# Performance work log

Hardware: AMD Instinct MI355X
Metric: run time of the kernel (lower is better)

## Reference

```python
import jax, jax.numpy as jnp
import numpy as np

B, P, E = 64, 196, 2048      # batch, num_pixels (14*14), encoder_size
H, EMB, V = 512, 512, 10000  # hidden_size, embed_size, vocab_size
T_CAP = 50                   # hard-coded pred/alpha buffer length
T_MAX = T_CAP - 1            # max(decode_lengths) = max(lengths) - 1 = 49


def setup_inputs() -> dict:
    key = jax.random.key(0)
    ks = jax.random.split(key, 20)

    def lin(k, out_f, in_f):
        kw, kb = jax.random.split(k)
        s = 1.0 / np.sqrt(in_f)
        return (jax.random.uniform(kw, (out_f, in_f), jnp.float32, -s, s),
                jax.random.uniform(kb, (out_f,), jnp.float32, -s, s))

    features = jax.random.normal(ks[0], (B, P, E), jnp.float32)
    captions = jax.random.randint(ks[1], (B, T_CAP), 0, V)
    # sorted descending, first length forced to 50 so max(decode_lengths)=49
    lengths = jnp.sort(jax.random.randint(ks[2], (B,), 2, T_CAP + 1))[::-1]
    lengths = lengths.at[0].set(T_CAP)

    Wx_w, Wx_b = lin(ks[3], E, E)          # attention Wx: encoder->encoder
    Wh_w, Wh_b = lin(ks[4], E, H)          # attention Wh: hidden->encoder
    V_w, V_b = lin(ks[5], 1, E)            # attention V: encoder->1
    init_h_w, init_h_b = lin(ks[6], H, E)  # init_h
    f_beta_w, f_beta_b = lin(ks[7], E, H)  # f_beta gate
    embed_w = jax.random.normal(ks[8], (V, EMB), jnp.float32)
    gru_w_ih, gru_b_ih = lin(ks[9], 3 * H, E + EMB)
    gru_w_hh, gru_b_hh = lin(ks[10], 3 * H, H)
    fc1_w, fc1_b = lin(ks[11], V, H)

    return dict(features=features, captions=captions, lengths=lengths,
                Wx_w=Wx_w, Wx_b=Wx_b, Wh_w=Wh_w, Wh_b=Wh_b, V_w=V_w, V_b=V_b,
                init_h_w=init_h_w, init_h_b=init_h_b,
                f_beta_w=f_beta_w, f_beta_b=f_beta_b, embed_w=embed_w,
                gru_w_ih=gru_w_ih, gru_b_ih=gru_b_ih,
                gru_w_hh=gru_w_hh, gru_b_hh=gru_b_hh,
                fc1_w=fc1_w, fc1_b=fc1_b)


def reference(features, captions, lengths, Wx_w, Wx_b, Wh_w, Wh_b, V_w, V_b,
              init_h_w, init_h_b, f_beta_w, f_beta_b, embed_w,
              gru_w_ih, gru_b_ih, gru_w_hh, gru_b_hh, fc1_w, fc1_b):
    b, p, e = features.shape
    vsz = fc1_w.shape[0]
    dec = lengths - 1                                  # decode_lengths
    # init hidden state from mean-pooled features
    h0 = jnp.mean(features, axis=1) @ init_h_w.T + init_h_b      # [B,H]
    # Wx(features) is time-invariant: precompute once
    x_wx = jnp.einsum('bpe,fe->bpf', features, Wx_w) + Wx_b      # [B,P,E]
    emb = embed_w[captions]                                      # [B,50,EMB]
    emb_t = jnp.transpose(emb[:, :T_MAX], (1, 0, 2))             # [T,B,EMB]

    def step(h, xs):
        t, e_t = xs
        active = (dec >= t)                            # rows still decoding
        # Bahdanau attention
        h_wh = h @ Wh_w.T + Wh_b                       # [B,E]
        lam = jnp.einsum('bpe,oe->bpo',
                         jnp.tanh(x_wx + h_wh[:, None, :]), V_w) + V_b
        alpha = jax.nn.softmax(lam, axis=1)            # [B,P,1]
        z = jnp.sum(alpha * features, axis=1)          # [B,E]
        # sigmoid gate
        gate = jax.nn.sigmoid(h @ f_beta_w.T + f_beta_b)
        inp = jnp.concatenate([gate * z, e_t], axis=1)  # [B,E+EMB]
        # GRUCell (torch gate order r,z,n)
        gi = inp @ gru_w_ih.T + gru_b_ih
        gh = h @ gru_w_hh.T + gru_b_hh
        i_r, i_z, i_n = jnp.split(gi, 3, axis=-1)
        h_r, h_z, h_n = jnp.split(gh, 3, axis=-1)
        r = jax.nn.sigmoid(i_r + h_r)
        zg = jax.nn.sigmoid(i_z + h_z)
        n = jnp.tanh(i_n + r * h_n)
        h_new = (1.0 - zg) * n + zg * h
        pred = h_new @ fc1_w.T + fc1_b                 # dropout in eval = id
        m = active[:, None]
        h_out = jnp.where(m, h_new, h)                 # freeze finished rows
        return h_out, (jnp.where(m, pred, 0.0),
                       jnp.where(m, alpha[..., 0], 0.0))

    _, (preds_t, alphas_t) = jax.lax.scan(
        step, h0, (jnp.arange(T_MAX), emb_t))
    preds = jnp.zeros((b, T_CAP, vsz), features.dtype)
    preds = preds.at[:, :T_MAX].set(jnp.transpose(preds_t, (1, 0, 2)))
    alphas = jnp.zeros((b, T_CAP, p), features.dtype)
    alphas = alphas.at[:, :T_MAX].set(jnp.transpose(alphas_t, (1, 0, 2)))
    return preds, alphas, dec
```

## Files before the change

### kernel.cpp

```cpp
#include <hip/hip_runtime.h>
#include <cstddef>

#define B_    64
#define P_    196
#define E_    2048
#define H_    512
#define EMB_  512
#define V_    10000
#define TCAP_ 50
#define TMAX_ 49
#define KI_   2560
#define G3_   1536

typedef __attribute__((ext_vector_type(8))) short short8;
typedef __attribute__((ext_vector_type(4))) float floatx4;
typedef unsigned int u32;
typedef const __attribute__((address_space(1))) u32* gptr_t;
typedef __attribute__((address_space(3))) u32* lptr_t;

__device__ __forceinline__ unsigned short f2bf_rne(float f) {
    unsigned int x = __float_as_uint(f);
    unsigned int r = (x + 0x7fffu + ((x >> 16) & 1u)) >> 16;
    return (unsigned short)r;
}
__device__ __forceinline__ float bf2f(unsigned int u16) {
    return __uint_as_float(u16 << 16);
}
__device__ __forceinline__ float fast_tanh(float x) {
    float a = fabsf(x);
    float e = __expf(2.0f * a);
    float r = 1.0f - 2.0f / (e + 1.0f);
    return (x < 0.0f) ? -r : r;
}
__device__ __forceinline__ float fast_sig(float x) {
    return 1.0f / (1.0f + __expf(-x));
}

__global__ void init_out_kernel(float* __restrict__ preds, float* __restrict__ alphas,
                                float* __restrict__ dec, const int* __restrict__ lens)
{
    int i = blockIdx.x * 256 + threadIdx.x;
    if (i < B_ * V_) {
        int b = i / V_, v = i - b * V_;
        preds[((size_t)b * TCAP_ + TMAX_) * V_ + v] = 0.f;
    }
    if (i < B_ * P_) {
        int b = i / P_, p = i - b * P_;
        alphas[((size_t)b * TCAP_ + TMAX_) * P_ + p] = 0.f;
    }
    if (i < B_) dec[i] = (float)(lens[i] - 1);
}

__global__ void f2bf_kernel(const float* __restrict__ src, unsigned short* __restrict__ dst, int n8)
{
    int i = blockIdx.x * 256 + threadIdx.x;
    if (i >= n8) return;
    float4 a = ((const float4*)src)[2 * i];
    float4 b = ((const float4*)src)[2 * i + 1];
    uint4 o;
    o.x = (unsigned)f2bf_rne(a.x) | ((unsigned)f2bf_rne(a.y) << 16);
    o.y = (unsigned)f2bf_rne(a.z) | ((unsigned)f2bf_rne(a.w) << 16);
    o.z = (unsigned)f2bf_rne(b.x) | ((unsigned)f2bf_rne(b.y) << 16);
    o.w = (unsigned)f2bf_rne(b.z) | ((unsigned)f2bf_rne(b.w) << 16);
    ((uint4*)dst)[i] = o;
}

__global__ void mean_kernel(const float* __restrict__ f, unsigned short* __restrict__ out)
{
    int i = blockIdx.x * 256 + threadIdx.x;
    int b = i >> 11, e = i & 2047;
    const float* p = f + (size_t)b * P_ * E_ + e;
    float s = 0.f;
    #pragma unroll 4
    for (int k = 0; k < P_; ++k) s += p[(size_t)k * E_];
    out[i] = f2bf_rne(s * (1.0f / (float)P_));
}

__global__ void __launch_bounds__(256)
mfma_xwx_kernel(const unsigned short* __restrict__ A,
                const unsigned short* __restrict__ W,
                const float* __restrict__ bias,
                unsigned short* __restrict__ C)
{
    __shared__ unsigned short As[128 * 64];
    __shared__ unsigned short Bs[128 * 64];
    int wv = threadIdx.x >> 6, lane = threadIdx.x & 63;
    int mr = lane & 15, quad = lane >> 4;
    int m0 = blockIdx.y * 128;
    int n0 = blockIdx.x * 128;
    int wm = (wv & 1) * 64, wn = (wv >> 1) * 64;
    int srow = wv * 32;
    int lrow = lane >> 3;
    int lcol = (lane & 7) * 8;
    floatx4 acc[4][4] = {};
    for (int k0 = 0; k0 < E_; k0 += 64) {
        __syncthreads();
        #pragma unroll
        for (int i = 0; i < 4; ++i) {
            int r = srow + i * 8;
            __builtin_amdgcn_global_load_lds(
                (gptr_t)(A + (size_t)(m0 + r + lrow) * E_ + k0 + lcol),
                (lptr_t)(As + r * 64), 16, 0, 0);
            __builtin_amdgcn_global_load_lds(
                (gptr_t)(W + (size_t)(n0 + r + lrow) * E_ + k0 + lcol),
                (lptr_t)(Bs + r * 64), 16, 0, 0);
        }
        __syncthreads();
        #pragma unroll
        for (int kk = 0; kk < 64; kk += 32) {
            short8 af[4], bf[4];
            #pragma unroll
            for (int i = 0; i < 4; ++i)
                af[i] = *(const short8*)(As + (wm + i * 16 + mr) * 64 + kk + quad * 8);
            #pragma unroll
            for (int j = 0; j < 4; ++j)
                bf[j] = *(const short8*)(Bs + (wn + j * 16 + mr) * 64 + kk + quad * 8);
            #pragma unroll
            for (int i = 0; i < 4; ++i)
                #pragma unroll
                for (int j = 0; j < 4; ++j)
                    acc[i][j] = __builtin_amdgcn_mfma_f32_16x16x32_bf16(af[i], bf[j], acc[i][j], 0, 0, 0);
        }
    }
    #pragma unroll
    for (int j = 0; j < 4; ++j) {
        int col = n0 + wn + j * 16 + mr;
        float bs = bias[col];
        #pragma unroll
        for (int i = 0; i < 4; ++i) {
            int row = m0 + wm + i * 16 + quad * 4;
            #pragma unroll
            for (int ii = 0; ii < 4; ++ii)
                C[(size_t)(row + ii) * E_ + col] = f2bf_rne(acc[i][j][ii] + bs);
        }
    }
}

template<int KC>
__global__ void __launch_bounds__(256)
mfma_gemm64(const unsigned short* __restrict__ A, int ld,
            const unsigned short* __restrict__ W,
            const float* __restrict__ bias,
            float* __restrict__ C, unsigned short* __restrict__ Cbf, int ldc)
{
    int wv = threadIdx.x >> 6, lane = threadIdx.x & 63;
    int mr = lane & 15, quad = lane >> 4;
    int m0 = wv * 16;
    int n0 = blockIdx.x * 16;
    const unsigned short* pa = A + (size_t)(m0 + mr) * ld + quad * 8;
    const unsigned short* pb = W + (size_t)(n0 + mr) * ld + quad * 8;
    floatx4 acc = {0.f, 0.f, 0.f, 0.f};
    #pragma unroll 16
    for (int k0 = 0; k0 < KC; k0 += 32) {
        short8 a = *(const short8*)(const void*)(pa + k0);
        short8 b = *(const short8*)(const void*)(pb + k0);
        acc = __builtin_amdgcn_mfma_f32_16x16x32_bf16(a, b, acc, 0, 0, 0);
    }
    int col = n0 + mr;
    float bs = bias ? bias[col] : 0.f;
    #pragma unroll
    for (int i = 0; i < 4; ++i) {
        int row = m0 + quad * 4 + i;
        float v = acc[i] + bs;
        C[(size_t)row * ldc + col] = v;
        if (Cbf) Cbf[(size_t)row * ldc + col] = f2bf_rne(v);
    }
}

__global__ void __launch_bounds__(256)
mfma_h3(const unsigned short* __restrict__ hbf,
        const unsigned short* __restrict__ whbf, const float* __restrict__ Wh_b,
        const unsigned short* __restrict__ fbbf, const float* __restrict__ fb_b,
        const unsigned short* __restrict__ ghhbf, const float* __restrict__ ghh_b,
        float* __restrict__ hwh, float* __restrict__ hf, float* __restrict__ gh)
{
    int bt = blockIdx.x;
    const unsigned short* W; const float* bias; float* C; int n0; int ldc;
    if (bt < 128)      { W = whbf;  bias = Wh_b;  C = hwh; n0 = bt * 16;         ldc = E_; }
    else if (bt < 256) { W = fbbf;  bias = fb_b;  C = hf;  n0 = (bt - 128) * 16; ldc = E_; }
    else               { W = ghhbf; bias = ghh_b; C = gh;  n0 = (bt - 256) * 16; ldc = G3_; }
    int wv = threadIdx.x >> 6, lane = threadIdx.x & 63;
    int mr = lane & 15, quad = lane >> 4;
    int m0 = wv * 16;
    const unsigned short* pa = hbf + (size_t)(m0 + mr) * H_ + quad * 8;
    const unsigned short* pb = W + (size_t)(n0 + mr) * H_ + quad * 8;
    floatx4 acc0 = {0.f, 0.f, 0.f, 0.f};
    floatx4 acc1 = {0.f, 0.f, 0.f, 0.f};
    #pragma unroll
    for (int k0 = 0; k0 < 256; k0 += 32) {
        short8 a0 = *(const short8*)(const void*)(pa + k0);
        short8 b0 = *(const short8*)(const void*)(pb + k0);
        acc0 = __builtin_amdgcn_mfma_f32_16x16x32_bf16(a0, b0, acc0, 0, 0, 0);
        short8 a1 = *(const short8*)(const void*)(pa + k0 + 256);
        short8 b1 = *(const short8*)(const void*)(pb + k0 + 256);
        acc1 = __builtin_amdgcn_mfma_f32_16x16x32_bf16(a1, b1, acc1, 0, 0, 0);
    }
    floatx4 acc = acc0 + acc1;
    int col = n0 + mr;
    float bs = bias[col];
    #pragma unroll
    for (int i = 0; i < 4; ++i) {
        int row = m0 + quad * 4 + i;
        C[(size_t)row * ldc + col] = acc[i] + bs;
    }
}

__global__ void __launch_bounds__(256)
lam_kernel(const unsigned short* __restrict__ xwx, const float* __restrict__ hwh,
           const float* __restrict__ Vw, const float* __restrict__ Vb,
           float* __restrict__ lam)
{
    __shared__ float sh[E_];
    __shared__ float sv[E_];
    int b = blockIdx.y;
    int p0 = blockIdx.x * 16;
    int tid = threadIdx.x;
    {
        const float4* hs = (const float4*)(hwh + (size_t)b * E_);
        const float4* vs = (const float4*)Vw;
        ((float4*)sh)[tid]       = hs[tid];
        ((float4*)sh)[tid + 256] = hs[tid + 256];
        ((float4*)sv)[tid]       = vs[tid];
        ((float4*)sv)[tid + 256] = vs[tid + 256];
    }
    __syncthreads();
    int wv = tid >> 6, lane = tid & 63;
    #pragma unroll
    for (int r = 0; r < 4; ++r) {
        int p = p0 + wv * 4 + r;
        if (p < P_) {
            const unsigned short* px = xwx + ((size_t)b * P_ + p) * E_;
            float acc = 0.f;
            #pragma unroll
            for (int it = 0; it < 4; ++it) {
                int e = it * 512 + lane * 8;
                uint4 u = *(const uint4*)(const void*)(px + e);
                float4 h0 = *(const float4*)(sh + e);
                float4 h1 = *(const float4*)(sh + e + 4);
                float4 v0 = *(const float4*)(sv + e);
                float4 v1 = *(const float4*)(sv + e + 4);
                acc = fmaf(fast_tanh(bf2f(u.x & 0xffffu) + h0.x), v0.x, acc);
                acc = fmaf(fast_tanh(bf2f(u.x >> 16)     + h0.y), v0.y, acc);
                acc = fmaf(fast_tanh(bf2f(u.y & 0xffffu) + h0.z), v0.z, acc);
                acc = fmaf(fast_tanh(bf2f(u.y >> 16)     + h0.w), v0.w, acc);
                acc = fmaf(fast_tanh(bf2f(u.z & 0xffffu) + h1.x), v1.x, acc);
                acc = fmaf(fast_tanh(bf2f(u.z >> 16)     + h1.y), v1.y, acc);
                acc = fmaf(fast_tanh(bf2f(u.w & 0xffffu) + h1.z), v1.z, acc);
                acc = fmaf(fast_tanh(bf2f(u.w >> 16)     + h1.w), v1.w, acc);
            }
            #pragma unroll
            for (int off = 32; off > 0; off >>= 1) acc += __shfl_down(acc, off);
            if (lane == 0) lam[b * P_ + p] = acc + Vb[0];
        }
    }
}

__global__ void __launch_bounds__(256)
attn_z_kernel(const unsigned short* __restrict__ fbf, const float* __restrict__ lam,
              const float* __restrict__ hf, const float* __restrict__ embed_w,
              const int* __restrict__ captions, const int* __restrict__ lens,
              unsigned short* __restrict__ inpbf, float* __restrict__ alphas, int t)
{
    int b = blockIdx.y;
    int tile = blockIdx.x;
    int tid = threadIdx.x;
    if (tile == 4) {
        int cap = captions[b * TCAP_ + t];
        const float* e = embed_w + (size_t)cap * EMB_;
        int c = tid * 2;
        float2 v = *(const float2*)(e + c);
        *(unsigned int*)(inpbf + (size_t)b * KI_ + E_ + c) =
            (unsigned)f2bf_rne(v.x) | ((unsigned)f2bf_rne(v.y) << 16);
        return;
    }
    __shared__ float sa[256];
    __shared__ float sr[256];
    float x = (tid < P_) ? lam[b * P_ + tid] : -1e30f;
    sr[tid] = x;
    __syncthreads();
    for (int s = 128; s > 0; s >>= 1) {
        if (tid < s) sr[tid] = fmaxf(sr[tid], sr[tid + s]);
        __syncthreads();
    }
    float mx = sr[0];
    __syncthreads();
    float ex = (tid < P_) ? __expf(x - mx) : 0.f;
    sa[tid] = ex;
    sr[tid] = ex;
    __syncthreads();
    for (int s = 128; s > 0; s >>= 1) {
        if (tid < s) sr[tid] += sr[tid + s];
        __syncthreads();
    }
    float inv = 1.0f / sr[0];
    if (tile == 0 && tid < P_) {
        alphas[(size_t)b * TCAP_ * P_ + (size_t)t * P_ + tid] = (lens[b] > t) ? ex * inv : 0.f;
    }
    int e0 = tile * 512 + tid * 2;
    const unsigned short* fp = fbf + (size_t)b * P_ * E_ + e0;
    float a0 = 0.f, a1 = 0.f;
    #pragma unroll 4
    for (int p = 0; p < P_; ++p) {
        unsigned int u = *(const unsigned int*)(const void*)(fp + (size_t)p * E_);
        float ap = sa[p];
        a0 = fmaf(ap, bf2f(u & 0xffffu), a0);
        a1 = fmaf(ap, bf2f(u >> 16), a1);
    }
    a0 *= inv; a1 *= inv;
    float2 gv = *(const float2*)(hf + (size_t)b * E_ + e0);
    float g0 = fast_sig(gv.x), g1 = fast_sig(gv.y);
    *(unsigned int*)(inpbf + (size_t)b * KI_ + e0) =
        (unsigned)f2bf_rne(g0 * a0) | ((unsigned)f2bf_rne(g1 * a1) << 16);
}

__global__ void __launch_bounds__(256)
gigru_kernel(const unsigned short* __restrict__ inpbf,
             const unsigned short* __restrict__ wihbf,
             const float* __restrict__ b_ih,
             const float* __restrict__ gh,
             const int* __restrict__ lens,
             float* __restrict__ h, unsigned short* __restrict__ hbf,
             unsigned short* __restrict__ Hall, int t)
{
    __shared__ float red[4][3][16][17];
    int wv = threadIdx.x >> 6, lane = threadIdx.x & 63;
    int mr = lane & 15, quad = lane >> 4;
    int j0 = blockIdx.x * 16;
    int m0 = blockIdx.y * 16;
    int koff = wv * 640;
    const unsigned short* pa = inpbf + (size_t)(m0 + mr) * KI_ + koff + quad * 8;
    const unsigned short* pb0 = wihbf + (size_t)(j0 + mr) * KI_ + koff + quad * 8;
    const unsigned short* pb1 = pb0 + (size_t)512 * KI_;
    const unsigned short* pb2 = pb0 + (size_t)1024 * KI_;
    floatx4 ar = {0.f,0.f,0.f,0.f}, az = {0.f,0.f,0.f,0.f}, an = {0.f,0.f,0.f,0.f};
    #pragma unroll 4
    for (int k0 = 0; k0 < 640; k0 += 32) {
        short8 a = *(const short8*)(const void*)(pa + k0);
        short8 br = *(const short8*)(const void*)(pb0 + k0);
        short8 bz = *(const short8*)(const void*)(pb1 + k0);
        short8 bn = *(const short8*)(const void*)(pb2 + k0);
        ar = __builtin_amdgcn_mfma_f32_16x16x32_bf16(a, br, ar, 0, 0, 0);
        az = __builtin_amdgcn_mfma_f32_16x16x32_bf16(a, bz, az, 0, 0, 0);
        an = __builtin_amdgcn_mfma_f32_16x16x32_bf16(a, bn, an, 0, 0, 0);
    }
    #pragma unroll
    for (int i = 0; i < 4; ++i) {
        red[wv][0][quad * 4 + i][mr] = ar[i];
        red[wv][1][quad * 4 + i][mr] = az[i];
        red[wv][2][quad * 4 + i][mr] = an[i];
    }
    __syncthreads();
    int row = threadIdx.x >> 4, col = threadIdx.x & 15;
    int b = m0 + row, j = j0 + col;
    float ir = red[0][0][row][col] + red[1][0][row][col] + red[2][0][row][col] + red[3][0][row][col] + b_ih[j];
    float iz = red[0][1][row][col] + red[1][1][row][col] + red[2][1][row][col] + red[3][1][row][col] + b_ih[512 + j];
    float in_= red[0][2][row][col] + red[1][2][row][col] + red[2][2][row][col] + red[3][2][row][col] + b_ih[1024 + j];
    float hr = gh[(size_t)b * G3_ + j];
    float hz = gh[(size_t)b * G3_ + 512 + j];
    float hn = gh[(size_t)b * G3_ + 1024 + j];
    float r  = fast_sig(ir + hr);
    float zg = fast_sig(iz + hz);
    float n  = fast_tanh(in_ + r * hn);
    float hp = h[(size_t)b * H_ + j];
    float hv = (1.f - zg) * n + zg * hp;
    float ho = (lens[b] > t) ? hv : hp;
    h[(size_t)b * H_ + j] = ho;
    unsigned short hob = f2bf_rne(ho);
    hbf[(size_t)b * H_ + j] = hob;
    Hall[((size_t)t * B_ + b) * H_ + j] = hob;
}

__global__ void __launch_bounds__(256)
fc1all_kernel(const unsigned short* __restrict__ Hall,
              const unsigned short* __restrict__ W,
              const float* __restrict__ bias,
              float* __restrict__ preds, const int* __restrict__ lens)
{
    int wv = threadIdx.x >> 6, lane = threadIdx.x & 63;
    int mr = lane & 15, quad = lane >> 4;
    int t = blockIdx.x;
    int m0 = t * 64 + wv * 16;
    int n0 = blockIdx.y * 64;
    const unsigned short* pa = Hall + (size_t)(m0 + mr) * H_ + quad * 8;
    const unsigned short* pw0 = W + (size_t)min(n0 + mr, V_ - 1) * H_ + quad * 8;
    const unsigned short* pw1 = W + (size_t)min(n0 + 16 + mr, V_ - 1) * H_ + quad * 8;
    const unsigned short* pw2 = W + (size_t)min(n0 + 32 + mr, V_ - 1) * H_ + quad * 8;
    const unsigned short* pw3 = W + (size_t)min(n0 + 48 + mr, V_ - 1) * H_ + quad * 8;
    floatx4 acc[4] = {{0.f,0.f,0.f,0.f},{0.f,0.f,0.f,0.f},{0.f,0.f,0.f,0.f},{0.f,0.f,0.f,0.f}};
    #pragma unroll
    for (int k0 = 0; k0 < H_; k0 += 32) {
        short8 a = *(const short8*)(const void*)(pa + k0);
        short8 b0 = *(const short8*)(const void*)(pw0 + k0);
        short8 b1 = *(const short8*)(const void*)(pw1 + k0);
        short8 b2 = *(const short8*)(const void*)(pw2 + k0);
        short8 b3 = *(const short8*)(const void*)(pw3 + k0);
        acc[0] = __builtin_amdgcn_mfma_f32_16x16x32_bf16(a, b0, acc[0], 0, 0, 0);
        acc[1] = __builtin_amdgcn_mfma_f32_16x16x32_bf16(a, b1, acc[1], 0, 0, 0);
        acc[2] = __builtin_amdgcn_mfma_f32_16x16x32_bf16(a, b2, acc[2], 0, 0, 0);
        acc[3] = __builtin_amdgcn_mfma_f32_16x16x32_bf16(a, b3, acc[3], 0, 0, 0);
    }
    #pragma unroll
    for (int r = 0; r < 4; ++r) {
        int col = n0 + r * 16 + mr;
        if (col >= V_) continue;
        float bs = bias[col];
        #pragma unroll
        for (int i = 0; i < 4; ++i) {
            int row = m0 + quad * 4 + i;
            int b = row - t * 64;
            float v = (lens[b] > t) ? (acc[r][i] + bs) : 0.f;
            preds[((size_t)b * TCAP_ + t) * V_ + col] = v;
        }
    }
}

extern "C" void kernel_launch(void* const* d_in, const int* in_sizes, int n_in,
                              void* d_out, int out_size, void* d_ws, size_t ws_size,
                              hipStream_t stream)
{
    const float* features  = (const float*)d_in[0];
    const int*   captions  = (const int*)d_in[1];
    const int*   lengths   = (const int*)d_in[2];
    const float* Wx_w      = (const float*)d_in[3];
    const float* Wx_b      = (const float*)d_in[4];
    const float* Wh_w      = (const float*)d_in[5];
    const float* Wh_b      = (const float*)d_in[6];
    const float* V_w       = (const float*)d_in[7];
    const float* V_b       = (const float*)d_in[8];
    const float* init_h_w  = (const float*)d_in[9];
    const float* init_h_b  = (const float*)d_in[10];
    const float* f_beta_w  = (const float*)d_in[11];
    const float* f_beta_b  = (const float*)d_in[12];
    const float* embed_w   = (const float*)d_in[13];
    const float* gru_w_ih  = (const float*)d_in[14];
    const float* gru_b_ih  = (const float*)d_in[15];
    const float* gru_w_hh  = (const float*)d_in[16];
    const float* gru_b_hh  = (const float*)d_in[17];
    const float* fc1_w     = (const float*)d_in[18];
    const float* fc1_b     = (const float*)d_in[19];

    float* preds  = (float*)d_out;
    float* alphas = preds + (size_t)B_ * TCAP_ * V_;
    float* dec    = alphas + (size_t)B_ * TCAP_ * P_;

    char* w = (char*)d_ws;
    unsigned short* fbf     = (unsigned short*)w; w += (size_t)12544 * 2048 * 2;
    unsigned short* xwx     = (unsigned short*)w; w += (size_t)12544 * 2048 * 2;
    unsigned short* wxbf    = (unsigned short*)w; w += (size_t)2048 * 2048 * 2;
    unsigned short* whbf    = (unsigned short*)w; w += (size_t)2048 * 512 * 2;
    unsigned short* fbbf    = (unsigned short*)w; w += (size_t)2048 * 512 * 2;
    unsigned short* ghhbf   = (unsigned short*)w; w += (size_t)1536 * 512 * 2;
    unsigned short* wihbf   = (unsigned short*)w; w += (size_t)1536 * 2560 * 2;
    unsigned short* fc1bf   = (unsigned short*)w; w += (size_t)10000 * 512 * 2;
    unsigned short* ihwbf   = (unsigned short*)w; w += (size_t)512 * 2048 * 2;
    unsigned short* fmeanbf = (unsigned short*)w; w += (size_t)64 * 2048 * 2;
    unsigned short* hbf     = (unsigned short*)w; w += (size_t)64 * 512 * 2;
    unsigned short* inpbf   = (unsigned short*)w; w += (size_t)64 * KI_ * 2;
    unsigned short* Hall    = (unsigned short*)w; w += (size_t)TMAX_ * 64 * 512 * 2;
    float* h   = (float*)w; w += (size_t)64 * 512 * 4;
    float* hwh = (float*)w; w += (size_t)64 * 2048 * 4;
    float* hf  = (float*)w; w += (size_t)64 * 2048 * 4;
    float* gh  = (float*)w; w += (size_t)64 * 1536 * 4;
    float* lam = (float*)w; w += (size_t)64 * 196 * 4;

    init_out_kernel<<<2500, 256, 0, stream>>>(preds, alphas, dec, lengths);

    f2bf_kernel<<<12544, 256, 0, stream>>>(features, fbf, 12544 * 2048 / 8);
    f2bf_kernel<<<2048, 256, 0, stream>>>(Wx_w, wxbf, 2048 * 2048 / 8);
    f2bf_kernel<<<512, 256, 0, stream>>>(Wh_w, whbf, 2048 * 512 / 8);
    f2bf_kernel<<<512, 256, 0, stream>>>(f_beta_w, fbbf, 2048 * 512 / 8);
    f2bf_kernel<<<384, 256, 0, stream>>>(gru_w_hh, ghhbf, 1536 * 512 / 8);
    f2bf_kernel<<<1920, 256, 0, stream>>>(gru_w_ih, wihbf, 1536 * 2560 / 8);
    f2bf_kernel<<<2500, 256, 0, stream>>>(fc1_w, fc1bf, 10000 * 512 / 8);
    f2bf_kernel<<<512, 256, 0, stream>>>(init_h_w, ihwbf, 512 * 2048 / 8);

    mean_kernel<<<512, 256, 0, stream>>>(features, fmeanbf);
    mfma_gemm64<2048><<<32, 256, 0, stream>>>(fmeanbf, 2048, ihwbf, init_h_b, h, hbf, 512);
    mfma_xwx_kernel<<<dim3(16, 98), 256, 0, stream>>>(fbf, wxbf, Wx_b, xwx);

    for (int t = 0; t < TMAX_; ++t) {
        mfma_h3<<<352, 256, 0, stream>>>(hbf, whbf, Wh_b, fbbf, f_beta_b, ghhbf, gru_b_hh,
                                         hwh, hf, gh);
        lam_kernel<<<dim3(13, 64), 256, 0, stream>>>(xwx, hwh, V_w, V_b, lam);
        attn_z_kernel<<<dim3(5, 64), 256, 0, stream>>>(fbf, lam, hf, embed_w, captions,
                                                       lengths, inpbf, alphas, t);
        gigru_kernel<<<dim3(32, 4), 256, 0, stream>>>(inpbf, wihbf, gru_b_ih, gh,
                                                      lengths, h, hbf, Hall, t);
    }
    fc1all_kernel<<<dim3(TMAX_, 157), 256, 0, stream>>>(Hall, fc1bf, fc1_b, preds, lengths);
}
```

Baseline: 4.016 ms.

## Tile fc1 GEMM through LDS and vectorize attention context reduction

Replaces the per-timestep fc1 output GEMM with a 128x128 LDS-tiled MFMA kernel. It stages Hall and fc1 weight tiles with global_load_lds and pads both buffers so out-of-range rows are never read past the allocation. Separately, attn_z now splits the 196 pixels across four waves, uses 16-byte loads of 8 bf16 values, and combines the partial sums through shared memory. Both changes aim to cut redundant global loads and raise memory efficiency. The risk is that the padded rows read whatever the workspace holds, and those values are masked only at the output store.

After: 3.328 ms. 17.1% less time.

```diff
diff --git a/kernel.cpp b/kernel.cpp
--- a/kernel.cpp
+++ b/kernel.cpp
@@ -136,6 +136,72 @@
     }
 }
 
+__global__ void __launch_bounds__(256)
+fc1tile_kernel(const unsigned short* __restrict__ Hall,
+               const unsigned short* __restrict__ W,
+               const float* __restrict__ bias,
+               float* __restrict__ preds, const int* __restrict__ lens)
+{
+    __shared__ unsigned short As[128 * 64];
+    __shared__ unsigned short Bs[128 * 64];
+    int wv = threadIdx.x >> 6, lane = threadIdx.x & 63;
+    int mr = lane & 15, quad = lane >> 4;
+    int m0 = blockIdx.y * 128;
+    int n0 = blockIdx.x * 128;
+    int wm = (wv & 1) * 64, wn = (wv >> 1) * 64;
+    int srow = wv * 32;
+    int lrow = lane >> 3;
+    int lcol = (lane & 7) * 8;
+    floatx4 acc[4][4] = {};
+    for (int k0 = 0; k0 < H_; k0 += 64) {
+        __syncthreads();
+        #pragma unroll
+        for (int i = 0; i < 4; ++i) {
+            int r = srow + i * 8;
+            __builtin_amdgcn_global_load_lds(
+                (gptr_t)(Hall + (size_t)(m0 + r + lrow) * H_ + k0 + lcol),
+                (lptr_t)(As + r * 64), 16, 0, 0);
+            __builtin_amdgcn_global_load_lds(
+                (gptr_t)(W + (size_t)(n0 + r + lrow) * H_ + k0 + lcol),
+                (lptr_t)(Bs + r * 64), 16, 0, 0);
+        }
+        __syncthreads();
+        #pragma unroll
+        for (int kk = 0; kk < 64; kk += 32) {
+            short8 af[4], bf[4];
+            #pragma unroll
+            for (int i = 0; i < 4; ++i)
+                af[i] = *(const short8*)(As + (wm + i * 16 + mr) * 64 + kk + quad * 8);
+            #pragma unroll
+            for (int j = 0; j < 4; ++j)
+                bf[j] = *(const short8*)(Bs + (wn + j * 16 + mr) * 64 + kk + quad * 8);
+            #pragma unroll
+            for (int i = 0; i < 4; ++i)
+                #pragma unroll
+                for (int j = 0; j < 4; ++j)
+                    acc[i][j] = __builtin_amdgcn_mfma_f32_16x16x32_bf16(af[i], bf[j], acc[i][j], 0, 0, 0);
+        }
+    }
+    #pragma unroll
+    for (int j = 0; j < 4; ++j) {
+        int col = n0 + wn + j * 16 + mr;
+        float bs = bias[min(col, V_ - 1)];
+        #pragma unroll
+        for (int i = 0; i < 4; ++i) {
+            int row = m0 + wm + i * 16 + quad * 4;
+            #pragma unroll
+            for (int ii = 0; ii < 4; ++ii) {
+                int r = row + ii;
+                if (r < TMAX_ * B_ && col < V_) {
+                    int t = r >> 6, b = r & 63;
+                    float v = (lens[b] > t) ? (acc[i][j][ii] + bs) : 0.f;
+                    preds[((size_t)b * TCAP_ + t) * V_ + col] = v;
+                }
+            }
+        }
+    }
+}
+
 template<int KC>
 __global__ void __launch_bounds__(256)
 mfma_gemm64(const unsigned short* __restrict__ A, int ld,
@@ -275,6 +341,7 @@
     }
     __shared__ float sa[256];
     __shared__ float sr[256];
+    __shared__ float psum[4][64][8];
     float x = (tid < P_) ? lam[b * P_ + tid] : -1e30f;
     sr[tid] = x;
     __syncthreads();
@@ -296,21 +363,39 @@
     if (tile == 0 && tid < P_) {
         alphas[(size_t)b * TCAP_ * P_ + (size_t)t * P_ + tid] = (lens[b] > t) ? ex * inv : 0.f;
     }
-    int e0 = tile * 512 + tid * 2;
-    const unsigned short* fp = fbf + (size_t)b * P_ * E_ + e0;
-    float a0 = 0.f, a1 = 0.f;
-    #pragma unroll 4
-    for (int p = 0; p < P_; ++p) {
-        unsigned int u = *(const unsigned int*)(const void*)(fp + (size_t)p * E_);
-        float ap = sa[p];
-        a0 = fmaf(ap, bf2f(u & 0xffffu), a0);
-        a1 = fmaf(ap, bf2f(u >> 16), a1);
-    }
-    a0 *= inv; a1 *= inv;
-    float2 gv = *(const float2*)(hf + (size_t)b * E_ + e0);
+    int wv = tid >> 6, lane = tid & 63;
+    int e0 = tile * 512;
+    const unsigned short* fp = fbf + ((size_t)b * P_ + wv * 49) * E_ + e0 + lane * 8;
+    float acc[8] = {0.f,0.f,0.f,0.f,0.f,0.f,0.f,0.f};
+    #pragma unroll 7
+    for (int i = 0; i < 49; ++i) {
+        uint4 u = *(const uint4*)(const void*)(fp + (size_t)i * E_);
+        float ap = sa[wv * 49 + i];
+        acc[0] = fmaf(ap, bf2f(u.x & 0xffffu), acc[0]);
+        acc[1] = fmaf(ap, bf2f(u.x >> 16),     acc[1]);
+        acc[2] = fmaf(ap, bf2f(u.y & 0xffffu), acc[2]);
+        acc[3] = fmaf(ap, bf2f(u.y >> 16),     acc[3]);
+        acc[4] = fmaf(ap, bf2f(u.z & 0xffffu), acc[4]);
+        acc[5] = fmaf(ap, bf2f(u.z >> 16),     acc[5]);
+        acc[6] = fmaf(ap, bf2f(u.w & 0xffffu), acc[6]);
+        acc[7] = fmaf(ap, bf2f(u.w >> 16),     acc[7]);
+    }
+    #pragma unroll
+    for (int k = 0; k < 8; ++k) psum[wv][lane][k] = acc[k];
+    __syncthreads();
+    int c0 = tid * 2;
+    int lc = c0 >> 3, kc = c0 & 7;
+    float2 s = {0.f, 0.f};
+    #pragma unroll
+    for (int w2 = 0; w2 < 4; ++w2) {
+        float2 v = *(const float2*)&psum[w2][lc][kc];
+        s.x += v.x; s.y += v.y;
+    }
+    s.x *= inv; s.y *= inv;
+    float2 gv = *(const float2*)(hf + (size_t)b * E_ + e0 + c0);
     float g0 = fast_sig(gv.x), g1 = fast_sig(gv.y);
-    *(unsigned int*)(inpbf + (size_t)b * KI_ + e0) =
-        (unsigned)f2bf_rne(g0 * a0) | ((unsigned)f2bf_rne(g1 * a1) << 16);
+    *(unsigned int*)(inpbf + (size_t)b * KI_ + e0 + c0) =
+        (unsigned)f2bf_rne(g0 * s.x) | ((unsigned)f2bf_rne(g1 * s.y) << 16);
 }
 
 __global__ void __launch_bounds__(256)
@@ -370,50 +455,6 @@
     Hall[((size_t)t * B_ + b) * H_ + j] = hob;
 }
 
-__global__ void __launch_bounds__(256)
-fc1all_kernel(const unsigned short* __restrict__ Hall,
-              const unsigned short* __restrict__ W,
-              const float* __restrict__ bias,
-              float* __restrict__ preds, const int* __restrict__ lens)
-{
-    int wv = threadIdx.x >> 6, lane = threadIdx.x & 63;
-    int mr = lane & 15, quad = lane >> 4;
-    int t = blockIdx.x;
-    int m0 = t * 64 + wv * 16;
-    int n0 = blockIdx.y * 64;
-    const unsigned short* pa = Hall + (size_t)(m0 + mr) * H_ + quad * 8;
-    const unsigned short* pw0 = W + (size_t)min(n0 + mr, V_ - 1) * H_ + quad * 8;
-    const unsigned short* pw1 = W + (size_t)min(n0 + 16 + mr, V_ - 1) * H_ + quad * 8;
-    const unsigned short* pw2 = W + (size_t)min(n0 + 32 + mr, V_ - 1) * H_ + quad * 8;
-    const unsigned short* pw3 = W + (size_t)min(n0 + 48 + mr, V_ - 1) * H_ + quad * 8;
-    floatx4 acc[4] = {{0.f,0.f,0.f,0.f},{0.f,0.f,0.f,0.f},{0.f,0.f,0.f,0.f},{0.f,0.f,0.f,0.f}};
-    #pragma unroll
-    for (int k0 = 0; k0 < H_; k0 += 32) {
-        short8 a = *(const short8*)(const void*)(pa + k0);
-        short8 b0 = *(const short8*)(const void*)(pw0 + k0);
-        short8 b1 = *(const short8*)(const void*)(pw1 + k0);
-        short8 b2 = *(const short8*)(const void*)(pw2 + k0);
-        short8 b3 = *(const short8*)(const void*)(pw3 + k0);
-        acc[0] = __builtin_amdgcn_mfma_f32_16x16x32_bf16(a, b0, acc[0], 0, 0, 0);
-        acc[1] = __builtin_amdgcn_mfma_f32_16x16x32_bf16(a, b1, acc[1], 0, 0, 0);
-        acc[2] = __builtin_amdgcn_mfma_f32_16x16x32_bf16(a, b2, acc[2], 0, 0, 0);
-        acc[3] = __builtin_amdgcn_mfma_f32_16x16x32_bf16(a, b3, acc[3], 0, 0, 0);
-    }
-    #pragma unroll
-    for (int r = 0; r < 4; ++r) {
-        int col = n0 + r * 16 + mr;
-        if (col >= V_) continue;
-        float bs = bias[col];
-        #pragma unroll
-        for (int i = 0; i < 4; ++i) {
-            int row = m0 + quad * 4 + i;
-            int b = row - t * 64;
-            float v = (lens[b] > t) ? (acc[r][i] + bs) : 0.f;
-            preds[((size_t)b * TCAP_ + t) * V_ + col] = v;
-        }
-    }
-}
-
 extern "C" void kernel_launch(void* const* d_in, const int* in_sizes, int n_in,
                               void* d_out, int out_size, void* d_ws, size_t ws_size,
                               hipStream_t stream)
@@ -451,12 +492,12 @@
     unsigned short* fbbf    = (unsigned short*)w; w += (size_t)2048 * 512 * 2;
     unsigned short* ghhbf   = (unsigned short*)w; w += (size_t)1536 * 512 * 2;
     unsigned short* wihbf   = (unsigned short*)w; w += (size_t)1536 * 2560 * 2;
-    unsigned short* fc1bf   = (unsigned short*)w; w += (size_t)10000 * 512 * 2;
+    unsigned short* fc1bf   = (unsigned short*)w; w += (size_t)10112 * 512 * 2;
     unsigned short* ihwbf   = (unsigned short*)w; w += (size_t)512 * 2048 * 2;
     unsigned short* fmeanbf = (unsigned short*)w; w += (size_t)64 * 2048 * 2;
     unsigned short* hbf     = (unsigned short*)w; w += (size_t)64 * 512 * 2;
     unsigned short* inpbf   = (unsigned short*)w; w += (size_t)64 * KI_ * 2;
-    unsigned short* Hall    = (unsigned short*)w; w += (size_t)TMAX_ * 64 * 512 * 2;
+    unsigned short* Hall    = (unsigned short*)w; w += (size_t)3200 * 512 * 2;
     float* h   = (float*)w; w += (size_t)64 * 512 * 4;
     float* hwh = (float*)w; w += (size_t)64 * 2048 * 4;
     float* hf  = (float*)w; w += (size_t)64 * 2048 * 4;
@@ -487,5 +528,5 @@
         gigru_kernel<<<dim3(32, 4), 256, 0, stream>>>(inpbf, wihbf, gru_b_ih, gh,
                                                       lengths, h, hbf, Hall, t);
     }
-    fc1all_kernel<<<dim3(TMAX_, 157), 256, 0, stream>>>(Hall, fc1bf, fc1_b, preds, lengths);
-}
+    fc1tile_kernel<<<dim3(79, 25), 256, 0, stream>>>(Hall, fc1bf, fc1_b, preds, lengths);
+}
```
